# Kernel tuning notes

Hardware: AMD Instinct MI355X
Metric: run time of the kernel (lower is better)

## Reference

```python
import jax, jax.numpy as jnp
import numpy as np

N, NFEAT, NHID, NCLASS, E = 100000, 128, 128, 40, 1600000

def _glorot(key, fan_in, fan_out):
    lim = float(np.sqrt(6.0 / (fan_in + fan_out)))
    return jax.random.uniform(key, (fan_in, fan_out), jnp.float32, -lim, lim)

def setup_inputs() -> dict:
    key = jax.random.key(0)
    ks = jax.random.split(key, 20)
    inp = {
        'x': jax.random.normal(ks[0], (N, NFEAT), jnp.float32),
        'edge_index': jax.random.randint(ks[1], (2, E), 0, N, jnp.int64 if jax.config.x64_enabled else jnp.int32),
    }
    dims = [(NFEAT, NHID), (NHID, NHID), (NHID, NHID), (NHID, NHID), (NHID, NHID), (NHID, NHID)]
    names = ['gc1_w1', 'gc1_w2', 'gc2_w1', 'gc2_w2', 'gc3_w1', 'gc3_w2']
    for i, (nm, (fi, fo)) in enumerate(zip(names, dims)):
        inp[nm] = _glorot(ks[2 + i], fi, fo)
        inp[nm.replace('w', 'b')] = jnp.zeros((fo,), jnp.float32)
    inp['lin1_w'] = _glorot(ks[10], 3 * NHID, 3 * NHID)
    inp['lin1_b'] = jnp.zeros((3 * NHID,), jnp.float32)
    inp['lin2_w'] = _glorot(ks[11], 3 * NHID, NCLASS)
    inp['lin2_b'] = jnp.zeros((NCLASS,), jnp.float32)
    return inp

def _gin_conv(x, src, dst, w1, b1, w2, b2):
    # GINConv, eps=0: mlp(x + sum_{j->i} x_j)
    agg = jax.ops.segment_sum(x[src], dst, num_segments=N)  # [N, d]
    h = jax.nn.relu((x + agg) @ w1 + b1)
    return jax.nn.relu(h @ w2 + b2)

def reference(x, edge_index, gc1_w1, gc1_b1, gc1_w2, gc1_b2,
              gc2_w1, gc2_b1, gc2_w2, gc2_b2,
              gc3_w1, gc3_b1, gc3_w2, gc3_b2,
              lin1_w, lin1_b, lin2_w, lin2_b):
    src, dst = edge_index[0], edge_index[1]
    h1 = _gin_conv(x, src, dst, gc1_w1, gc1_b1, gc1_w2, gc1_b2)
    h2 = _gin_conv(h1, src, dst, gc2_w1, gc2_b1, gc2_w2, gc2_b2)
    h3 = _gin_conv(h2, src, dst, gc3_w1, gc3_b1, gc3_w2, gc3_b2)
    h = jnp.concatenate([h1, h2, h3], axis=1)  # [N, 3*nhid]
    h = jax.nn.relu(h @ lin1_w + lin1_b)  # dropout inactive in eval mode
    h = h @ lin2_w + lin2_b
    return jax.nn.log_softmax(h, axis=1)
```

## Files before the change

### kernel.cpp

```cpp
#include <hip/hip_runtime.h>

#define N_NODES 100000
#define NEDGE   1600000
#define NHID    128
#define NCLASS  40

#define AGG_NODES 128
#define COLV_LDS  3072
#define FILL_SLICES 8
#define FILL_RANGE  12500
#define WPREP_TOT   264192

using bf16x8 = __attribute__((ext_vector_type(8))) short;
using f32x4  = __attribute__((ext_vector_type(4))) float;

__device__ __forceinline__ float bf2f(unsigned short s) {
    unsigned u = ((unsigned)s) << 16; float f; __builtin_memcpy(&f, &u, 4); return f;
}
__device__ __forceinline__ unsigned short f2bf(float f) {
    unsigned u; __builtin_memcpy(&u, &f, 4);
    u = u + 0x7fffu + ((u >> 16) & 1u);
    return (unsigned short)(u >> 16);
}

__device__ __forceinline__ void gld16(const void* g, void* l) {
    __builtin_amdgcn_global_load_lds(g, l, 16, 0, 0);
}

__global__ __launch_bounds__(256) void k_countr(const int* __restrict__ ei, int* __restrict__ cnt) {
    int slice = blockIdx.x & 7;
    int e = (blockIdx.x >> 3) * 256 + threadIdx.x;
    if (e >= NEDGE) return;
    int d = __builtin_nontemporal_load(ei + NEDGE + e);
    int lo = slice * FILL_RANGE;
    if (d >= lo && d < lo + FILL_RANGE) atomicAdd(&cnt[d], 1);
}

__global__ void k_scan1(const int* __restrict__ cnt, int* __restrict__ rp, int* __restrict__ bsum) {
    __shared__ int sh[256];
    int t = threadIdx.x, base = blockIdx.x * 1024;
    int v[4]; int s = 0;
    for (int k = 0; k < 4; ++k) { int i = base + t * 4 + k; v[k] = (i < N_NODES) ? cnt[i] : 0; s += v[k]; }
    sh[t] = s; __syncthreads();
    for (int off = 1; off < 256; off <<= 1) {
        int x = (t >= off) ? sh[t - off] : 0;
        __syncthreads();
        sh[t] += x;
        __syncthreads();
    }
    int excl = sh[t] - s;
    for (int k = 0; k < 4; ++k) { int i = base + t * 4 + k; if (i < N_NODES) rp[i] = excl; excl += v[k]; }
    if (t == 255) bsum[blockIdx.x] = sh[255];
}

__global__ void k_scan2(int* __restrict__ bsum, int nb) {
    __shared__ int sh[256];
    int t = threadIdx.x;
    int v = (t < nb) ? bsum[t] : 0;
    sh[t] = v; __syncthreads();
    for (int off = 1; off < 256; off <<= 1) {
        int x = (t >= off) ? sh[t - off] : 0;
        __syncthreads();
        sh[t] += x;
        __syncthreads();
    }
    if (t < nb) bsum[t] = sh[t] - v;
}

__global__ void k_scan3(int* __restrict__ rp, const int* __restrict__ bsum, int* __restrict__ cur) {
    int base = blockIdx.x * 1024;
    int off = bsum[blockIdx.x];
    for (int k = 0; k < 4; ++k) {
        int i = base + threadIdx.x * 4 + k;
        if (i < N_NODES) { int v = rp[i] + off; rp[i] = v; cur[i] = v; }
    }
    if (blockIdx.x == 0 && threadIdx.x == 0) rp[N_NODES] = NEDGE;
}

__global__ __launch_bounds__(256) void k_fillr(const int* __restrict__ ei,
                                               int* __restrict__ cur, int* __restrict__ colv) {
    int slice = blockIdx.x & 7;
    int e = (blockIdx.x >> 3) * 256 + threadIdx.x;
    if (e >= NEDGE) return;
    int d = __builtin_nontemporal_load(ei + NEDGE + e);
    int lo = slice * FILL_RANGE;
    if (d >= lo && d < lo + FILL_RANGE) {
        int p = atomicAdd(&cur[d], 1);
        colv[p] = __builtin_nontemporal_load(ei + e);
    }
}

__global__ void k_wprep_all(const float* __restrict__ g0, const float* __restrict__ g1,
                            const float* __restrict__ g2, const float* __restrict__ g3,
                            const float* __restrict__ g4, const float* __restrict__ g5,
                            const float* __restrict__ l1w, const float* __restrict__ l2w,
                            unsigned short* __restrict__ dst) {
    int idx = blockIdx.x * 256 + threadIdx.x;
    if (idx >= WPREP_TOT) return;
    const float* w; int local, K, O;
    if (idx < 98304) {
        int r = idx >> 14; local = idx & 16383; K = 128; O = 128;
        w = r == 0 ? g0 : r == 1 ? g1 : r == 2 ? g2 : r == 3 ? g3 : r == 4 ? g4 : g5;
    } else if (idx < 245760) {
        local = idx - 98304; K = 384; O = 384; w = l1w;
    } else {
        local = idx - 245760; K = 384; O = 40; w = l2w;
    }
    int kss = K >> 5;
    int e = local & 7, lane = (local >> 3) & 63, rest = local >> 9;
    int ks = rest % kss, ot = rest / kss;
    int c = ot * 16 + (lane & 15);
    int k = ks * 32 + (lane >> 4) * 8 + e;
    float v = (c < O) ? w[k * O + c] : 0.f;
    dst[idx] = f2bf(v);
}

__global__ void k_xprep(const float* __restrict__ x, unsigned short* __restrict__ xs) {
    int s = blockIdx.x & 3;
    int rest = (blockIdx.x >> 2) * 256 + threadIdx.x;
    if (rest >= N_NODES * 16) return;
    int n = rest >> 4, wrd = rest & 15;
    float2 v = *(const float2*)(x + (size_t)n * 128 + s * 32 + wrd * 2);
    ((unsigned*)xs)[(size_t)s * N_NODES * 16 + rest] =
        (unsigned)f2bf(v.x) | ((unsigned)f2bf(v.y) << 16);
}

__device__ __forceinline__ void acc8(float* acc, uint4 f, float m) {
    unsigned u[4] = {f.x, f.y, f.z, f.w};
    for (int d = 0; d < 4; ++d) {
        acc[2 * d]     = fmaf(m, bf2f((unsigned short)u[d]), acc[2 * d]);
        acc[2 * d + 1] = fmaf(m, bf2f((unsigned short)(u[d] >> 16)), acc[2 * d + 1]);
    }
}

__global__ __launch_bounds__(512) void k_aggs(const unsigned short* __restrict__ feat,
                                              unsigned short* __restrict__ tout,
                                              const int* __restrict__ rp,
                                              const int* __restrict__ colv) {
    __shared__ int scol[COLV_LDS + 8];
    __shared__ int srp[AGG_NODES + 1];
    const int s = blockIdx.x & 3;
    const int chunk = blockIdx.x >> 2;
    const int tid = threadIdx.x;
    const int nbase = chunk * AGG_NODES;

    for (int i = tid; i <= AGG_NODES; i += 512) {
        int n = nbase + i;
        srp[i] = rp[n <= N_NODES ? n : N_NODES];
    }
    __syncthreads();
    const int ebase = srp[0];
    const int ecount = srp[AGG_NODES] - ebase;
    const int elds = ecount < COLV_LDS ? ecount : COLV_LDS;
    for (int i = tid; i < elds; i += 512) scol[i] = colv[ebase + i];
    if (tid < 8) scol[elds + tid] = 0;
    __syncthreads();

    const unsigned* fs = (const unsigned*)feat + (size_t)s * N_NODES * 16;
    unsigned* ts = (unsigned*)tout + (size_t)s * N_NODES * 16;

    const int sub = tid >> 2, q = tid & 3;
    const int node = nbase + sub;
    if (node >= N_NODES) return;
    const int off = q * 4;
    const int e0 = srp[sub] - ebase, e1 = srp[sub + 1] - ebase;

    float acc[8];
    {
        uint4 a = *(const uint4*)(fs + (size_t)node * 16 + off);
        unsigned u[4] = {a.x, a.y, a.z, a.w};
        for (int d = 0; d < 4; ++d) {
            acc[2 * d]     = bf2f((unsigned short)u[d]);
            acc[2 * d + 1] = bf2f((unsigned short)(u[d] >> 16));
        }
    }

    if (ecount <= COLV_LDS) {
        int e = e0;
        const int efull = e0 + ((e1 - e0) & ~7);
        for (; e < efull; e += 8) {
            int j[8];
            #pragma unroll
            for (int k = 0; k < 8; ++k) j[k] = scol[e + k];
            uint4 f[8];
            #pragma unroll
            for (int k = 0; k < 8; ++k)
                f[k] = *(const uint4*)(fs + (size_t)j[k] * 16 + off);
            #pragma unroll
            for (int k = 0; k < 8; ++k) acc8(acc, f[k], 1.f);
        }
        if (e < e1) {
            int j[8]; float m[8];
            #pragma unroll
            for (int k = 0; k < 8; ++k) {
                int ee = e + k;
                bool v = ee < e1;
                j[k] = v ? scol[ee] : node;
                m[k] = v ? 1.f : 0.f;
            }
            uint4 f[8];
            #pragma unroll
            for (int k = 0; k < 8; ++k)
                f[k] = *(const uint4*)(fs + (size_t)j[k] * 16 + off);
            #pragma unroll
            for (int k = 0; k < 8; ++k) acc8(acc, f[k], m[k]);
        }
    } else {
        for (int e = e0; e < e1; e += 8) {
            int j[8]; float m[8];
            #pragma unroll
            for (int k = 0; k < 8; ++k) {
                int ee = e + k;
                bool v = ee < e1;
                int idx = ee < COLV_LDS ? scol[ee] : colv[ebase + ee];
                j[k] = v ? idx : node;
                m[k] = v ? 1.f : 0.f;
            }
            uint4 f[8];
            #pragma unroll
            for (int k = 0; k < 8; ++k)
                f[k] = *(const uint4*)(fs + (size_t)j[k] * 16 + off);
            #pragma unroll
            for (int k = 0; k < 8; ++k) acc8(acc, f[k], m[k]);
        }
    }

    uint4 o;
    o.x = (unsigned)f2bf(acc[0]) | ((unsigned)f2bf(acc[1]) << 16);
    o.y = (unsigned)f2bf(acc[2]) | ((unsigned)f2bf(acc[3]) << 16);
    o.z = (unsigned)f2bf(acc[4]) | ((unsigned)f2bf(acc[5]) << 16);
    o.w = (unsigned)f2bf(acc[6]) | ((unsigned)f2bf(acc[7]) << 16);
    *(uint4*)(ts + (size_t)node * 16 + off) = o;
}

__global__ __launch_bounds__(512) void k_mlp(
    const unsigned short* __restrict__ tin,
    const unsigned short* __restrict__ w1t, const float* __restrict__ b1,
    const unsigned short* __restrict__ w2t, const float* __restrict__ b2,
    unsigned short* __restrict__ hout) {
    __shared__ __align__(16) char tlds[4 * 8192];
    __shared__ __align__(16) char hlds[4 * 8192];
    const int tid = threadIdx.x, lane = tid & 63, w = tid >> 6;
    const int l15 = lane & 15, lg = lane >> 4;
    const int nbase = blockIdx.x * 128;
    const int rx = (l15 >> 1) & 3;

    #pragma unroll
    for (int i = 0; i < 4; ++i) {
        int c = w + i * 8;
        int s = c >> 3, rblk = c & 7;
        int node = nbase + rblk * 16 + (lane >> 2);
        if (node >= N_NODES) node = 0;
        int hsrc = (lane & 3) ^ ((lane >> 3) & 3);
        gld16(tin + ((size_t)s * N_NODES + node) * 32 + hsrc * 8,
              tlds + c * 1024);
    }

    bf16x8 B1[4], B2[4];
    const int col = w * 16 + l15;
    const float bias1 = b1[col], bias2 = b2[col];
    #pragma unroll
    for (int ks = 0; ks < 4; ++ks) {
        B1[ks] = *(const bf16x8*)(w1t + ((size_t)(w * 4 + ks) * 64 + lane) * 8);
        B2[ks] = *(const bf16x8*)(w2t + ((size_t)(w * 4 + ks) * 64 + lane) * 8);
    }
    __syncthreads();

    {
        const int hoff = ((lg ^ rx) << 4);
        bf16x8 A[2][4];
        #pragma unroll
        for (int ks = 0; ks < 4; ++ks)
            A[0][ks] = *(const bf16x8*)(tlds + ks * 8192 + l15 * 64 + hoff);
        #pragma unroll
        for (int m = 0; m < 8; ++m) {
            int cur = m & 1, nxt = cur ^ 1;
            if (m < 7) {
                int row = (m + 1) * 16 + l15;
                #pragma unroll
                for (int ks = 0; ks < 4; ++ks)
                    A[nxt][ks] = *(const bf16x8*)(tlds + ks * 8192 + row * 64 + hoff);
            }
            f32x4 acc = {0.f, 0.f, 0.f, 0.f};
            #pragma unroll
            for (int ks = 0; ks < 4; ++ks)
                acc = __builtin_amdgcn_mfma_f32_16x16x32_bf16(A[cur][ks], B1[ks], acc, 0, 0, 0);
            #pragma unroll
            for (int r = 0; r < 4; ++r) {
                int row = m * 16 + lg * 4 + r;
                int rw = (2 * lg + (r >> 1)) & 3;
                int h = (w & 1) * 2 + (l15 >> 3);
                float v = acc[r] + bias1; v = v > 0.f ? v : 0.f;
                *(unsigned short*)(hlds + (w >> 1) * 8192 + row * 64 +
                                   ((h ^ rw) << 4) + (l15 & 7) * 2) = f2bf(v);
            }
        }
    }
    __syncthreads();

    {
        const int hoff = ((lg ^ rx) << 4);
        bf16x8 A[2][4];
        #pragma unroll
        for (int ks = 0; ks < 4; ++ks)
            A[0][ks] = *(const bf16x8*)(hlds + ks * 8192 + l15 * 64 + hoff);
        #pragma unroll
        for (int m = 0; m < 8; ++m) {
            int cur = m & 1, nxt = cur ^ 1;
            if (m < 7) {
                int row = (m + 1) * 16 + l15;
                #pragma unroll
                for (int ks = 0; ks < 4; ++ks)
                    A[nxt][ks] = *(const bf16x8*)(hlds + ks * 8192 + row * 64 + hoff);
            }
            f32x4 acc = {0.f, 0.f, 0.f, 0.f};
            #pragma unroll
            for (int ks = 0; ks < 4; ++ks)
                acc = __builtin_amdgcn_mfma_f32_16x16x32_bf16(A[cur][ks], B2[ks], acc, 0, 0, 0);
            #pragma unroll
            for (int r = 0; r < 4; ++r) {
                int node = nbase + m * 16 + lg * 4 + r;
                if (node < N_NODES) {
                    float v = acc[r] + bias2; v = v > 0.f ? v : 0.f;
                    hout[((size_t)(w >> 1) * N_NODES + node) * 32 + (w & 1) * 16 + l15] = f2bf(v);
                }
            }
        }
    }
}

__global__ __launch_bounds__(512, 4) void k_final(
    const unsigned short* __restrict__ h1, const unsigned short* __restrict__ h2,
    const unsigned short* __restrict__ h3,
    const unsigned short* __restrict__ l1t, const float* __restrict__ l1b,
    const unsigned short* __restrict__ l2t, const float* __restrict__ l2b,
    float* __restrict__ out) {
    __shared__ __align__(16) char lds[12 * 4096];
    const int tid = threadIdx.x, lane = tid & 63, w = tid >> 6;
    const int l15 = lane & 15, lg = lane >> 4;
    const int nbase = blockIdx.x * 64;
    const int rx = (l15 >> 1) & 3;

    #pragma unroll
    for (int i = 0; i < 6; ++i) {
        int c = w + i * 8;
        int g = c >> 2, rblk = c & 3;
        int part = g >> 2, slice = g & 3;
        int node = nbase + rblk * 16 + (lane >> 2);
        if (node >= N_NODES) node = 0;
        int hsrc = (lane & 3) ^ ((lane >> 3) & 3);
        const unsigned short* hp = part == 0 ? h1 : (part == 1 ? h2 : h3);
        gld16(hp + ((size_t)slice * N_NODES + node) * 32 + hsrc * 8,
              lds + c * 1024);
    }

    bf16x8 B[2][3];
    #pragma unroll
    for (int ot = 0; ot < 3; ++ot)
        B[0][ot] = *(const bf16x8*)(l1t + ((size_t)((w * 3 + ot) * 12) * 64 + lane) * 8);
    __syncthreads();

    f32x4 acc[4][3];
    #pragma unroll
    for (int m = 0; m < 4; ++m)
        #pragma unroll
        for (int ot = 0; ot < 3; ++ot) acc[m][ot] = {0.f, 0.f, 0.f, 0.f};
    {
        const int hoff = ((lg ^ rx) << 4);
        #pragma unroll
        for (int ks = 0; ks < 12; ++ks) {
            int cur = ks & 1, nxt = cur ^ 1;
            if (ks < 11) {
                #pragma unroll
                for (int ot = 0; ot < 3; ++ot)
                    B[nxt][ot] = *(const bf16x8*)(l1t + ((size_t)((w * 3 + ot) * 12 + ks + 1) * 64 + lane) * 8);
            }
            bf16x8 A[4];
            #pragma unroll
            for (int m = 0; m < 4; ++m) {
                int row = m * 16 + l15;
                A[m] = *(const bf16x8*)(lds + ks * 4096 + row * 64 + hoff);
            }
            #pragma unroll
            for (int ot = 0; ot < 3; ++ot)
                #pragma unroll
                for (int m = 0; m < 4; ++m)
                    acc[m][ot] = __builtin_amdgcn_mfma_f32_16x16x32_bf16(A[m], B[cur][ot], acc[m][ot], 0, 0, 0);
        }
    }
    __syncthreads();

    #pragma unroll
    for (int ot = 0; ot < 3; ++ot) {
        int c = (w * 3 + ot) * 16 + l15;
        int gc = c >> 5, h = (c >> 3) & 3, b2i = (c & 7) * 2;
        float bias = l1b[c];
        #pragma unroll
        for (int m = 0; m < 4; ++m)
            #pragma unroll
            for (int r = 0; r < 4; ++r) {
                int row = m * 16 + lg * 4 + r;
                int rw = (2 * lg + (r >> 1)) & 3;
                float v = acc[m][ot][r] + bias; v = v > 0.f ? v : 0.f;
                *(unsigned short*)(lds + gc * 4096 + row * 64 + ((h ^ rw) << 4) + b2i) = f2bf(v);
            }
    }
    __syncthreads();

    if (w < 4) {
        f32x4 acc2[3];
        #pragma unroll
        for (int ot = 0; ot < 3; ++ot) acc2[ot] = {0.f, 0.f, 0.f, 0.f};
        {
            const int row = w * 16 + l15;
            const int hoff = ((lg ^ rx) << 4);
            bf16x8 C2[2][3];
            #pragma unroll
            for (int ot = 0; ot < 3; ++ot)
                C2[0][ot] = *(const bf16x8*)(l2t + ((size_t)(ot * 12) * 64 + lane) * 8);
            #pragma unroll
            for (int ks = 0; ks < 12; ++ks) {
                int cur = ks & 1, nxt = cur ^ 1;
                if (ks < 11) {
                    #pragma unroll
                    for (int ot = 0; ot < 3; ++ot)
                        C2[nxt][ot] = *(const bf16x8*)(l2t + ((size_t)(ot * 12 + ks + 1) * 64 + lane) * 8);
                }
                bf16x8 A2 = *(const bf16x8*)(lds + ks * 4096 + row * 64 + hoff);
                #pragma unroll
                for (int ot = 0; ot < 3; ++ot)
                    acc2[ot] = __builtin_amdgcn_mfma_f32_16x16x32_bf16(A2, C2[cur][ot], acc2[ot], 0, 0, 0);
            }
        }

        int c0 = l15;
        #pragma unroll
        for (int r = 0; r < 4; ++r) {
            float v0 = acc2[0][r] + l2b[c0];
            float v1 = acc2[1][r] + l2b[c0 + 16];
            float v2 = (c0 < 8) ? (acc2[2][r] + l2b[c0 + 32]) : -1e30f;
            float mx = fmaxf(fmaxf(v0, v1), v2);
            for (int msk = 1; msk < 16; msk <<= 1) mx = fmaxf(mx, __shfl_xor(mx, msk));
            float s = __expf(v0 - mx) + __expf(v1 - mx) + ((c0 < 8) ? __expf(v2 - mx) : 0.f);
            for (int msk = 1; msk < 16; msk <<= 1) s += __shfl_xor(s, msk);
            float lse = mx + __logf(s);
            int node = nbase + w * 16 + lg * 4 + r;
            if (node < N_NODES) {
                out[(size_t)node * 40 + c0] = v0 - lse;
                out[(size_t)node * 40 + c0 + 16] = v1 - lse;
                if (c0 < 8) out[(size_t)node * 40 + c0 + 32] = v2 - lse;
            }
        }
    }
}

extern "C" void kernel_launch(void* const* d_in, const int* in_sizes, int n_in,
                              void* d_out, int out_size, void* d_ws, size_t ws_size,
                              hipStream_t stream) {
    const float* x  = (const float*)d_in[0];
    const int*   ei = (const int*)d_in[1];
    const float* gw1[3] = {(const float*)d_in[2],  (const float*)d_in[6],  (const float*)d_in[10]};
    const float* gb1[3] = {(const float*)d_in[3],  (const float*)d_in[7],  (const float*)d_in[11]};
    const float* gw2[3] = {(const float*)d_in[4],  (const float*)d_in[8],  (const float*)d_in[12]};
    const float* gb2[3] = {(const float*)d_in[5],  (const float*)d_in[9],  (const float*)d_in[13]};
    const float* l1w = (const float*)d_in[14];
    const float* l1b = (const float*)d_in[15];
    const float* l2w = (const float*)d_in[16];
    const float* l2b = (const float*)d_in[17];
    float* out = (float*)d_out;

    char* p = (char*)d_ws;
    auto alloc = [&](size_t bytes) { char* q = p; p += (bytes + 255) & ~(size_t)255; return q; };
    int* rp   = (int*)alloc(4 * (N_NODES + 1));
    int* cnt  = (int*)alloc(4 * N_NODES);
    int* cur  = (int*)alloc(4 * N_NODES);
    int* bsum = (int*)alloc(4 * 256);
    int* colv = (int*)alloc(4 * (size_t)NEDGE);
    unsigned short* t  = (unsigned short*)alloc(2 * (size_t)N_NODES * 128);
    unsigned short* h1 = (unsigned short*)alloc(2 * (size_t)N_NODES * 128);
    unsigned short* h2 = (unsigned short*)alloc(2 * (size_t)N_NODES * 128);
    unsigned short* h3 = (unsigned short*)alloc(2 * (size_t)N_NODES * 128);
    unsigned short* xs = h3;
    unsigned short* wt[6];
    for (int i = 0; i < 6; ++i) wt[i] = (unsigned short*)alloc(2 * 128 * 128);
    unsigned short* l1t = (unsigned short*)alloc(2 * 384 * 384);
    unsigned short* l2t = (unsigned short*)alloc(2 * 48 * 384);

    const int nb = (N_NODES + 1023) / 1024;
    hipMemsetAsync(cnt, 0, 4 * N_NODES, stream);
    k_countr<<<((NEDGE + 255) / 256) * FILL_SLICES, 256, 0, stream>>>(ei, cnt);
    k_scan1<<<nb, 256, 0, stream>>>(cnt, rp, bsum);
    k_scan2<<<1, 256, 0, stream>>>(bsum, nb);
    k_scan3<<<nb, 256, 0, stream>>>(rp, bsum, cur);
    k_fillr<<<((NEDGE + 255) / 256) * FILL_SLICES, 256, 0, stream>>>(ei, cur, colv);

    k_wprep_all<<<(WPREP_TOT + 255) / 256, 256, 0, stream>>>(
        gw1[0], gw2[0], gw1[1], gw2[1], gw1[2], gw2[2], l1w, l2w, wt[0]);

    k_xprep<<<4 * ((N_NODES * 16 + 255) / 256), 256, 0, stream>>>(x, xs);

    const int gagg = ((N_NODES + AGG_NODES - 1) / AGG_NODES) * 4;
    const int gtile2 = (N_NODES + 127) / 128;
    const int gtile1 = (N_NODES + 63) / 64;
    k_aggs<<<gagg, 512, 0, stream>>>(xs, t, rp, colv);
    k_mlp<<<gtile2, 512, 0, stream>>>(t, wt[0], gb1[0], wt[1], gb2[0], h1);
    k_aggs<<<gagg, 512, 0, stream>>>(h1, t, rp, colv);
    k_mlp<<<gtile2, 512, 0, stream>>>(t, wt[2], gb1[1], wt[3], gb2[1], h2);
    k_aggs<<<gagg, 512, 0, stream>>>(h2, t, rp, colv);
    k_mlp<<<gtile2, 512, 0, stream>>>(t, wt[4], gb1[2], wt[5], gb2[2], h3);
    k_final<<<gtile1, 512, 0, stream>>>(h1, h2, h3, l1t, l1b, l2t, l2b, out);
}
```

Measured before the change: 481.7 us.

## Pre-bucket edges by destination slice before CSR count and fill

Replaces the sliced count/fill passes, which each re-read the whole edge list eight times and filtered by destination range, with a bucketing pass. Edges are packed into (local dst, src) words grouped by slice. The count and fill kernels then scan only their slice's contiguous range, so edge-list reads drop and atomics stay localized per slice. This adds two small kernels, a memset and an extra pairs buffer. Packing src into 17 bits holds only while N stays below 131072.

```diff
diff --git a/kernel.cpp b/kernel.cpp
--- a/kernel.cpp
+++ b/kernel.cpp
@@ -10,6 +10,8 @@
 #define FILL_SLICES 8
 #define FILL_RANGE  12500
 #define WPREP_TOT   264192
+#define EPB 2048
+#define C2B 128
 
 using bf16x8 = __attribute__((ext_vector_type(8))) short;
 using f32x4  = __attribute__((ext_vector_type(4))) float;
@@ -27,13 +29,62 @@
     __builtin_amdgcn_global_load_lds(g, l, 16, 0, 0);
 }
 
-__global__ __launch_bounds__(256) void k_countr(const int* __restrict__ ei, int* __restrict__ cnt) {
-    int slice = blockIdx.x & 7;
-    int e = (blockIdx.x >> 3) * 256 + threadIdx.x;
-    if (e >= NEDGE) return;
-    int d = __builtin_nontemporal_load(ei + NEDGE + e);
-    int lo = slice * FILL_RANGE;
-    if (d >= lo && d < lo + FILL_RANGE) atomicAdd(&cnt[d], 1);
+__global__ __launch_bounds__(256) void k_slicecnt(const int* __restrict__ ei, int* __restrict__ meta) {
+    __shared__ int h[8];
+    int tid = threadIdx.x;
+    if (tid < 8) h[tid] = 0;
+    __syncthreads();
+    int e = blockIdx.x * 256 + tid;
+    if (e < NEDGE) atomicAdd(&h[ei[NEDGE + e] / FILL_RANGE], 1);
+    __syncthreads();
+    if (tid < 8 && h[tid]) atomicAdd(&meta[tid], h[tid]);
+}
+
+__global__ void k_prefix8(int* __restrict__ meta) {
+    if (threadIdx.x == 0 && blockIdx.x == 0) {
+        int run = 0;
+        for (int i = 0; i < 8; ++i) { meta[8 + i] = run; meta[17 + i] = run; run += meta[i]; }
+        meta[16] = run;
+    }
+}
+
+__global__ __launch_bounds__(256) void k_bucket(const int* __restrict__ ei, int* __restrict__ meta,
+                                                unsigned* __restrict__ pairs) {
+    __shared__ int lcnt[8], base[8], lpos[8];
+    const int tid = threadIdx.x;
+    const int e0 = blockIdx.x * EPB;
+    if (tid < 8) { lcnt[tid] = 0; lpos[tid] = 0; }
+    __syncthreads();
+    int d[8], s[8], sl[8];
+    #pragma unroll
+    for (int k = 0; k < 8; ++k) {
+        int e = e0 + k * 256 + tid;
+        bool v = e < NEDGE;
+        d[k] = v ? ei[NEDGE + e] : 0;
+        s[k] = v ? ei[e] : 0;
+        sl[k] = v ? d[k] / FILL_RANGE : -1;
+        if (v) atomicAdd(&lcnt[sl[k]], 1);
+    }
+    __syncthreads();
+    if (tid < 8) base[tid] = atomicAdd(&meta[17 + tid], lcnt[tid]);
+    __syncthreads();
+    #pragma unroll
+    for (int k = 0; k < 8; ++k) {
+        if (sl[k] >= 0) {
+            int pos = atomicAdd(&lpos[sl[k]], 1);
+            int dl = d[k] - sl[k] * FILL_RANGE;
+            pairs[base[sl[k]] + pos] = ((unsigned)dl << 17) | (unsigned)s[k];
+        }
+    }
+}
+
+__global__ __launch_bounds__(256) void k_count2(const unsigned* __restrict__ pairs,
+                                                const int* __restrict__ meta, int* __restrict__ cnt) {
+    int s = blockIdx.x & 7, b = blockIdx.x >> 3;
+    int lo = s * FILL_RANGE;
+    int beg = meta[8 + s], end = meta[8 + s + 1];
+    for (int i = beg + b * 256 + threadIdx.x; i < end; i += C2B * 256)
+        atomicAdd(&cnt[lo + (int)(pairs[i] >> 17)], 1);
 }
 
 __global__ void k_scan1(const int* __restrict__ cnt, int* __restrict__ rp, int* __restrict__ bsum) {
@@ -77,16 +128,17 @@
     if (blockIdx.x == 0 && threadIdx.x == 0) rp[N_NODES] = NEDGE;
 }
 
-__global__ __launch_bounds__(256) void k_fillr(const int* __restrict__ ei,
+__global__ __launch_bounds__(256) void k_fill2(const unsigned* __restrict__ pairs,
+                                               const int* __restrict__ meta,
                                                int* __restrict__ cur, int* __restrict__ colv) {
-    int slice = blockIdx.x & 7;
-    int e = (blockIdx.x >> 3) * 256 + threadIdx.x;
-    if (e >= NEDGE) return;
-    int d = __builtin_nontemporal_load(ei + NEDGE + e);
-    int lo = slice * FILL_RANGE;
-    if (d >= lo && d < lo + FILL_RANGE) {
-        int p = atomicAdd(&cur[d], 1);
-        colv[p] = __builtin_nontemporal_load(ei + e);
+    int s = blockIdx.x & 7, b = blockIdx.x >> 3;
+    int lo = s * FILL_RANGE;
+    int beg = meta[8 + s], end = meta[8 + s + 1];
+    for (int i = beg + b * 256 + threadIdx.x; i < end; i += C2B * 256) {
+        unsigned p = pairs[i];
+        int d = lo + (int)(p >> 17);
+        int q = atomicAdd(&cur[d], 1);
+        colv[q] = (int)(p & 0x1FFFFu);
     }
 }
 
@@ -471,11 +523,13 @@
 
     char* p = (char*)d_ws;
     auto alloc = [&](size_t bytes) { char* q = p; p += (bytes + 255) & ~(size_t)255; return q; };
-    int* rp   = (int*)alloc(4 * (N_NODES + 1));
-    int* cnt  = (int*)alloc(4 * N_NODES);
-    int* cur  = (int*)alloc(4 * N_NODES);
-    int* bsum = (int*)alloc(4 * 256);
-    int* colv = (int*)alloc(4 * (size_t)NEDGE);
+    int* rp    = (int*)alloc(4 * (N_NODES + 1));
+    int* cnt   = (int*)alloc(4 * N_NODES);
+    int* cur   = (int*)alloc(4 * N_NODES);
+    int* bsum  = (int*)alloc(4 * 256);
+    int* meta  = (int*)alloc(4 * 32);
+    unsigned* pairs = (unsigned*)alloc(4 * (size_t)NEDGE);
+    int* colv  = (int*)alloc(4 * (size_t)NEDGE);
     unsigned short* t  = (unsigned short*)alloc(2 * (size_t)N_NODES * 128);
     unsigned short* h1 = (unsigned short*)alloc(2 * (size_t)N_NODES * 128);
     unsigned short* h2 = (unsigned short*)alloc(2 * (size_t)N_NODES * 128);
@@ -488,11 +542,15 @@
 
     const int nb = (N_NODES + 1023) / 1024;
     hipMemsetAsync(cnt, 0, 4 * N_NODES, stream);
-    k_countr<<<((NEDGE + 255) / 256) * FILL_SLICES, 256, 0, stream>>>(ei, cnt);
+    hipMemsetAsync(meta, 0, 4 * 32, stream);
+    k_slicecnt<<<(NEDGE + 255) / 256, 256, 0, stream>>>(ei, meta);
+    k_prefix8<<<1, 64, 0, stream>>>(meta);
+    k_bucket<<<(NEDGE + EPB - 1) / EPB, 256, 0, stream>>>(ei, meta, pairs);
+    k_count2<<<8 * C2B, 256, 0, stream>>>(pairs, meta, cnt);
     k_scan1<<<nb, 256, 0, stream>>>(cnt, rp, bsum);
     k_scan2<<<1, 256, 0, stream>>>(bsum, nb);
     k_scan3<<<nb, 256, 0, stream>>>(rp, bsum, cur);
-    k_fillr<<<((NEDGE + 255) / 256) * FILL_SLICES, 256, 0, stream>>>(ei, cur, colv);
+    k_fill2<<<8 * C2B, 256, 0, stream>>>(pairs, meta, cur, colv);
 
     k_wprep_all<<<(WPREP_TOT + 255) / 256, 256, 0, stream>>>(
         gw1[0], gw2[0], gw1[1], gw2[1], gw1[2], gw2[2], l1w, l2w, wt[0]);
```

Result: slower. 560.1 us (+16.3%).
